# Kernel optimization log

Hardware: AMD Instinct MI355X
Metric: run time of the kernel (lower is better)

Reference implementation:

```python
import jax, jax.numpy as jnp
import numpy as np

B, N, D = 2, 2048, 1024   # batch, seq, input_dim
H, DK, DV = 8, 128, 1024  # heads, qk_dim, v_dim (v_dim == input_dim for residual)


def setup_inputs() -> dict:
    key = jax.random.key(0)
    kx, kq, kk, kv = jax.random.split(key, 4)
    scale = 0.02
    x = jax.random.normal(kx, (B, N, D), dtype=jnp.float32)
    # torch nn.Linear weights are [out_features, in_features]; stacked over heads.
    Wq = jax.random.normal(kq, (H, DK, D), dtype=jnp.float32) * scale
    Wk = jax.random.normal(kk, (H, DK, D), dtype=jnp.float32) * scale
    Wv = jax.random.normal(kv, (H, DV, D), dtype=jnp.float32) * scale
    return {"x": x, "Wq": Wq, "Wk": Wk, "Wv": Wv}


def reference(x, Wq, Wk, Wv):
    # x: [B, N, D]; Wq/Wk: [H, DK, D]; Wv: [H, DV, D]
    n = x.shape[-2]
    Q = jnp.einsum('bnd,hed->bhne', x, Wq)  # [B,H,N,DK]
    K = jnp.einsum('bnd,hed->bhne', x, Wk)  # [B,H,N,DK]
    V = jnp.einsum('bnd,hvd->bhnv', x, Wv)  # [B,H,N,DV]
    scores = jnp.einsum('bhne,bhme->bhnm', Q, K)  # [B,H,N,N]
    # causal mask: masked entries set to mask_value=0.0, then relu, then /N
    causal = jnp.tril(jnp.ones((n, n), dtype=bool))
    sim = jnp.where(causal, jax.nn.relu(scores), jnp.float32(0.0)) / jnp.float32(n)
    # sum of per-head outputs added to residual
    head_out = jnp.einsum('bhnm,bhmv->bnv', sim, V)  # [B,N,DV]
    return x + head_out
```

## Files before the change

kernel.cpp:

```cpp
#include <hip/hip_runtime.h>

typedef __attribute__((ext_vector_type(8))) short bf16x8;
typedef __attribute__((ext_vector_type(4))) float floatx4;

__device__ __forceinline__ unsigned short f2bf(float f) {
  unsigned int u = __builtin_bit_cast(unsigned int, f);
  unsigned int r = (u + 0x7fffu + ((u >> 16) & 1u)) >> 16;
  return (unsigned short)r;
}

__device__ __forceinline__ unsigned int pack2(float a, float b) {
  return (unsigned int)f2bf(a) | ((unsigned int)f2bf(b) << 16);
}

__device__ __forceinline__ void gload16(const void* g, void* l) {
  __builtin_amdgcn_global_load_lds(
      (__attribute__((address_space(1))) void*)g,
      (__attribute__((address_space(3))) void*)l, 16, 0, 0);
}

__device__ __forceinline__ void barrier_lgkm() {
  asm volatile("s_waitcnt lgkmcnt(0)" ::: "memory");
  __builtin_amdgcn_s_barrier();
  __builtin_amdgcn_sched_barrier(0);
}

__global__ __launch_bounds__(256) void init_out(const float4* __restrict__ x,
                                                float4* __restrict__ out, int n4) {
  for (int i = blockIdx.x * 256 + threadIdx.x; i < n4; i += gridDim.x * 256)
    out[i] = x[i];
}

__global__ __launch_bounds__(256) void convert_all(
    const float4* __restrict__ x4,
    const float4* __restrict__ wq4, const float4* __restrict__ wk4,
    const float4* __restrict__ wv4,
    uint2* __restrict__ xb4, uint2* __restrict__ wqkb4, uint2* __restrict__ wvb4)
{
  const int NX = 2 * 2048 * 1024 / 4;
  const int NQK = 8 * 256 * 1024 / 4;
  const int NV = 8 * 1024 * 1024 / 4;
  const int total = NX + NQK + NV;
  const float inv_n = 1.0f / 2048.0f;
  for (int i = blockIdx.x * 256 + threadIdx.x; i < total; i += gridDim.x * 256) {
    float4 f; uint2* dst;
    if (i < NX) {
      f = x4[i]; dst = &xb4[i];
    } else if (i < NX + NQK) {
      int j = i - NX;
      int c = j & 255;
      int row = j >> 8;
      int h = row >> 8, r = row & 255;
      f = (r < 128) ? wq4[(h * 128 + r) * 256 + c] : wk4[(h * 128 + r - 128) * 256 + c];
      dst = &wqkb4[j];
    } else {
      int j = i - NX - NQK;
      f = wv4[j];
      f.x *= inv_n; f.y *= inv_n; f.z *= inv_n; f.w *= inv_n;
      dst = &wvb4[j];
    }
    uint2 p; p.x = pack2(f.x, f.y); p.y = pack2(f.z, f.w);
    *dst = p;
  }
}

__global__ __launch_bounds__(256) void gemm_bf16_bt(
    const unsigned short* __restrict__ Abase, long sAb, long sAh,
    const unsigned short* __restrict__ Bbase, long sBb, long sBh,
    unsigned short* __restrict__ C0base, long sC0, int ld0,
    unsigned short* __restrict__ C1base, long sC1, int ld1,
    int split, int K)
{
  const int z = blockIdx.z;
  const int b = z >> 3, h = z & 7;
  const unsigned short* Ag = Abase + (long)b * sAb + (long)h * sAh + (long)blockIdx.x * 128 * K;
  const unsigned short* Bg = Bbase + (long)b * sBb + (long)h * sBh + (long)blockIdx.y * 128 * K;
  __shared__ __align__(16) unsigned short LA[128 * 64];
  __shared__ __align__(16) unsigned short LB[128 * 64];
  const int t = threadIdx.x;
  const int l = t & 63, w = t >> 6;
  const int wr = w >> 1, wc = w & 1;
  const int l16 = l & 15, lq = l >> 4;
  floatx4 acc[4][4] = {};
  for (int k0 = 0; k0 < K; k0 += 64) {
    __syncthreads();
    for (int i = 0; i < 4; i++) {
      int cbase = i * 256 + (t & 192);
      int chunk = cbase + (t & 63);
      int row = chunk >> 3, c8 = chunk & 7;
      gload16(Ag + (long)row * K + k0 + c8 * 8, &LA[cbase * 8]);
      gload16(Bg + (long)row * K + k0 + c8 * 8, &LB[cbase * 8]);
    }
    __syncthreads();
    for (int kk = 0; kk < 2; kk++) {
      bf16x8 af[4], bfr[4];
      for (int m = 0; m < 4; m++)
        af[m]  = *reinterpret_cast<const bf16x8*>(&LA[(wr * 64 + m * 16 + l16) * 64 + kk * 32 + lq * 8]);
      for (int n = 0; n < 4; n++)
        bfr[n] = *reinterpret_cast<const bf16x8*>(&LB[(wc * 64 + n * 16 + l16) * 64 + kk * 32 + lq * 8]);
      for (int m = 0; m < 4; m++)
        for (int n = 0; n < 4; n++)
          acc[m][n] = __builtin_amdgcn_mfma_f32_16x16x32_bf16(af[m], bfr[n], acc[m][n], 0, 0, 0);
    }
  }
  unsigned short* C0 = C0base + (long)z * sC0;
  unsigned short* C1 = C1base + (long)z * sC1;
  for (int m = 0; m < 4; m++)
    for (int n = 0; n < 4; n++)
      for (int j = 0; j < 4; j++) {
        int row = blockIdx.x * 128 + wr * 64 + m * 16 + lq * 4 + j;
        int col = blockIdx.y * 128 + wc * 64 + n * 16 + l16;
        unsigned short v = f2bf(acc[m][n][j]);
        if (col < split) C0[(long)row * ld0 + col] = v;
        else             C1[(long)row * ld1 + (col - split)] = v;
      }
}

__global__ __launch_bounds__(256) void gemm_bt(
    const float* __restrict__ Abase, long sAb, long sAh,
    const float* __restrict__ Bbase, long sBb, long sBh,
    unsigned short* __restrict__ Cbase, long sC,
    int M, int Nc, int K, int H, float cscale)
{
  int z = blockIdx.z;
  int b = z / H, h = z % H;
  const float* A  = Abase + (long)b * sAb + (long)h * sAh;
  const float* Bm = Bbase + (long)b * sBb + (long)h * sBh;
  unsigned short* C = Cbase + (long)z * sC;
  int tRow = blockIdx.x * 128;
  int tCol = blockIdx.y * 128;
  __shared__ __align__(16) unsigned short LA[128 * 72];
  __shared__ __align__(16) unsigned short LB[128 * 72];
  int t = threadIdx.x;
  int l = t & 63, w = t >> 6;
  int wr = w >> 1, wc = w & 1;
  int l16 = l & 15, lq = l >> 4;
  floatx4 acc[4][4] = {};
  for (int k0 = 0; k0 < K; k0 += 64) {
    __syncthreads();
    for (int i = 0; i < 8; i++) {
      int lin = i * 256 + t;
      int row = lin >> 4;
      int c4  = lin & 15;
      float4 va = *reinterpret_cast<const float4*>(A + (long)(tRow + row) * K + k0 + c4 * 4);
      uint2 pa; pa.x = pack2(va.x, va.y); pa.y = pack2(va.z, va.w);
      *reinterpret_cast<uint2*>(&LA[row * 72 + c4 * 4]) = pa;
      float4 vb = *reinterpret_cast<const float4*>(Bm + (long)(tCol + row) * K + k0 + c4 * 4);
      uint2 pb; pb.x = pack2(vb.x, vb.y); pb.y = pack2(vb.z, vb.w);
      *reinterpret_cast<uint2*>(&LB[row * 72 + c4 * 4]) = pb;
    }
    __syncthreads();
    for (int kk = 0; kk < 2; kk++) {
      bf16x8 af[4], bfr[4];
      for (int m = 0; m < 4; m++)
        af[m]  = *reinterpret_cast<const bf16x8*>(&LA[(wr * 64 + m * 16 + l16) * 72 + kk * 32 + lq * 8]);
      for (int n = 0; n < 4; n++)
        bfr[n] = *reinterpret_cast<const bf16x8*>(&LB[(wc * 64 + n * 16 + l16) * 72 + kk * 32 + lq * 8]);
      for (int m = 0; m < 4; m++)
        for (int n = 0; n < 4; n++)
          acc[m][n] = __builtin_amdgcn_mfma_f32_16x16x32_bf16(af[m], bfr[n], acc[m][n], 0, 0, 0);
    }
  }
  for (int m = 0; m < 4; m++)
    for (int n = 0; n < 4; n++)
      for (int j = 0; j < 4; j++) {
        int row = tRow + wr * 64 + m * 16 + lq * 4 + j;
        int col = tCol + wc * 64 + n * 16 + l16;
        C[(long)row * Nc + col] = f2bf(acc[m][n][j] * cscale);
      }
}

__global__ __launch_bounds__(256) void gemm_qk(
    const float* __restrict__ x,
    const float* __restrict__ Wq, const float* __restrict__ Wk,
    unsigned short* __restrict__ Qb, unsigned short* __restrict__ Kb)
{
  int z = blockIdx.z;
  int b = z >> 3, h = z & 7;
  const float* A  = x + (long)b * 2048 * 1024;
  const float* Bm = (blockIdx.y ? Wk : Wq) + (long)h * 128 * 1024;
  unsigned short* C = (blockIdx.y ? Kb : Qb) + (long)z * 2048 * 128;
  int tRow = blockIdx.x * 128;
  __shared__ __align__(16) unsigned short LA[128 * 72];
  __shared__ __align__(16) unsigned short LB[128 * 72];
  int t = threadIdx.x;
  int l = t & 63, w = t >> 6;
  int wr = w >> 1, wc = w & 1;
  int l16 = l & 15, lq = l >> 4;
  floatx4 acc[4][4] = {};
  const int K = 1024;
  for (int k0 = 0; k0 < K; k0 += 64) {
    __syncthreads();
    for (int i = 0; i < 8; i++) {
      int lin = i * 256 + t;
      int row = lin >> 4;
      int c4  = lin & 15;
      float4 va = *reinterpret_cast<const float4*>(A + (long)(tRow + row) * K + k0 + c4 * 4);
      uint2 pa; pa.x = pack2(va.x, va.y); pa.y = pack2(va.z, va.w);
      *reinterpret_cast<uint2*>(&LA[row * 72 + c4 * 4]) = pa;
      float4 vb = *reinterpret_cast<const float4*>(Bm + (long)row * K + k0 + c4 * 4);
      uint2 pb; pb.x = pack2(vb.x, vb.y); pb.y = pack2(vb.z, vb.w);
      *reinterpret_cast<uint2*>(&LB[row * 72 + c4 * 4]) = pb;
    }
    __syncthreads();
    for (int kk = 0; kk < 2; kk++) {
      bf16x8 af[4], bfr[4];
      for (int m = 0; m < 4; m++)
        af[m]  = *reinterpret_cast<const bf16x8*>(&LA[(wr * 64 + m * 16 + l16) * 72 + kk * 32 + lq * 8]);
      for (int n = 0; n < 4; n++)
        bfr[n] = *reinterpret_cast<const bf16x8*>(&LB[(wc * 64 + n * 16 + l16) * 72 + kk * 32 + lq * 8]);
      for (int m = 0; m < 4; m++)
        for (int n = 0; n < 4; n++)
          acc[m][n] = __builtin_amdgcn_mfma_f32_16x16x32_bf16(af[m], bfr[n], acc[m][n], 0, 0, 0);
    }
  }
  for (int m = 0; m < 4; m++)
    for (int n = 0; n < 4; n++)
      for (int j = 0; j < 4; j++) {
        int row = tRow + wr * 64 + m * 16 + lq * 4 + j;
        int col = wc * 64 + n * 16 + l16;
        C[(long)row * 128 + col] = f2bf(acc[m][n][j]);
      }
}

__global__ __launch_bounds__(256) void attn_fused(
    const unsigned short* __restrict__ Qb,
    const unsigned short* __restrict__ Kb,
    const unsigned short* __restrict__ Vtb,
    float* __restrict__ out)
{
  const int z = blockIdx.z;
  const int b = z >> 3;
  const int pair = blockIdx.y;
  const int vb = blockIdx.x;
  const int t = threadIdx.x;
  const int l = t & 63, w = t >> 6;
  const int l16 = l & 15, lq = l >> 4;
  const int wm = w & 1, wn = w >> 1;
  const int swz = l16 & 7;

  __shared__ __align__(16) unsigned short LK[64 * 128];
  __shared__ __align__(16) unsigned short LV[128 * 64];
  __shared__ __align__(16) unsigned short LP[64 * 64];

  const unsigned short* Qz = Qb + (long)z * 2048 * 128;
  const unsigned short* Kh = Kb + (long)z * 2048 * 128;
  const unsigned short* Vh = Vtb + (long)z * 1024 * 2048 + (long)(vb * 128) * 2048;

  int koff[4], voff[4];
  unsigned short *pK[4], *pV[4];
#pragma unroll
  for (int i = 0; i < 4; i++) {
    int lin = i * 256 + t;
    int r = lin >> 4, c = lin & 15;
    koff[i] = r * 128 + c * 8;
    pK[i] = &LK[r * 128 + ((((c & 7) ^ (r & 7)) | (c & 8)) * 8)];
    int rv = lin >> 3, cv = lin & 7;
    voff[i] = rv * 2048 + cv * 8;
    pV[i] = &LV[rv * 64 + ((cv ^ (rv & 7)) * 8)];
  }

  for (int hf = 0; hf < 2; hf++) {
    const int T = hf ? (31 - pair) : pair;
    const unsigned short* Qh = Qz + (long)T * 64 * 128;
    bf16x8 aQ[2][4];
#pragma unroll
    for (int sn = 0; sn < 2; sn++)
#pragma unroll
      for (int ke = 0; ke < 4; ke++)
        aQ[sn][ke] = *reinterpret_cast<const bf16x8*>(
            Qh + (long)(wn * 32 + sn * 16 + l16) * 128 + ke * 32 + lq * 8);
    floatx4 acc[4][2] = {};
    for (int M = 0; M <= T; M++) {
      uint4 ks[4], vs[4];
#pragma unroll
      for (int i = 0; i < 4; i++) {
        ks[i] = *reinterpret_cast<const uint4*>(Kh + M * 8192 + koff[i]);
        vs[i] = *reinterpret_cast<const uint4*>(Vh + M * 64 + voff[i]);
      }
      barrier_lgkm();
#pragma unroll
      for (int i = 0; i < 4; i++) {
        *reinterpret_cast<uint4*>(pK[i]) = ks[i];
        *reinterpret_cast<uint4*>(pV[i]) = vs[i];
      }
      barrier_lgkm();
      floatx4 sacc[2][2] = {{{}, {}}, {{}, {}}};
      __builtin_amdgcn_s_setprio(1);
#pragma unroll
      for (int ke = 0; ke < 4; ke++) {
        bf16x8 kf[2];
#pragma unroll
        for (int sm = 0; sm < 2; sm++) {
          int chunk = 4 * ke + lq;
          kf[sm] = *reinterpret_cast<const bf16x8*>(
              &LK[(wm * 32 + sm * 16 + l16) * 128 +
                  ((((chunk & 7) ^ swz) | (chunk & 8)) * 8)]);
        }
#pragma unroll
        for (int sm = 0; sm < 2; sm++)
#pragma unroll
          for (int sn = 0; sn < 2; sn++)
            sacc[sm][sn] = __builtin_amdgcn_mfma_f32_16x16x32_bf16(
                kf[sm], aQ[sn][ke], sacc[sm][sn], 0, 0, 0);
      }
      __builtin_amdgcn_s_setprio(0);
      const bool diag = (M == T);
#pragma unroll
      for (int sm = 0; sm < 2; sm++)
#pragma unroll
        for (int sn = 0; sn < 2; sn++) {
          floatx4 v = sacc[sm][sn];
          float f0 = fmaxf(v[0], 0.0f), f1 = fmaxf(v[1], 0.0f);
          float f2 = fmaxf(v[2], 0.0f), f3 = fmaxf(v[3], 0.0f);
          if (diag) {
            int mm = wm * 32 + sm * 16 + lq * 4;
            int nn = wn * 32 + sn * 16 + l16;
            if (mm + 0 > nn) f0 = 0.0f;
            if (mm + 1 > nn) f1 = 0.0f;
            if (mm + 2 > nn) f2 = 0.0f;
            if (mm + 3 > nn) f3 = 0.0f;
          }
          unsigned int p0, p1;
          asm("v_cvt_pk_bf16_f32 %0, %1, %2" : "=v"(p0) : "v"(f0), "v"(f1));
          asm("v_cvt_pk_bf16_f32 %0, %1, %2" : "=v"(p1) : "v"(f2), "v"(f3));
          uint2 pk; pk.x = p0; pk.y = p1;
          int row = wn * 32 + sn * 16 + l16;
          int cs = wm * 32 + sm * 16 + lq * 4;
          *reinterpret_cast<uint2*>(
              &LP[row * 64 + (((cs >> 3) ^ (row & 7)) * 8) + (cs & 7)]) = pk;
        }
      barrier_lgkm();
      __builtin_amdgcn_s_setprio(1);
#pragma unroll
      for (int km = 0; km < 2; km++) {
        bf16x8 aP[4], bV[2];
#pragma unroll
        for (int nf = 0; nf < 4; nf++)
          aP[nf] = *reinterpret_cast<const bf16x8*>(
              &LP[(nf * 16 + l16) * 64 + (((4 * km + lq) ^ swz) * 8)]);
#pragma unroll
        for (int vf = 0; vf < 2; vf++)
          bV[vf] = *reinterpret_cast<const bf16x8*>(
              &LV[(w * 32 + vf * 16 + l16) * 64 + (((4 * km + lq) ^ swz) * 8)]);
#pragma unroll
        for (int nf = 0; nf < 4; nf++)
#pragma unroll
          for (int vf = 0; vf < 2; vf++)
            acc[nf][vf] = __builtin_amdgcn_mfma_f32_16x16x32_bf16(
                aP[nf], bV[vf], acc[nf][vf], 0, 0, 0);
      }
      __builtin_amdgcn_s_setprio(0);
    }
#pragma unroll
    for (int nf = 0; nf < 4; nf++)
#pragma unroll
      for (int vf = 0; vf < 2; vf++)
#pragma unroll
        for (int j = 0; j < 4; j++) {
          int n = T * 64 + nf * 16 + lq * 4 + j;
          int v = vb * 128 + w * 32 + vf * 16 + l16;
          long idx = ((long)b * 2048 + n) * 1024 + v;
          unsafeAtomicAdd(&out[idx], acc[nf][vf][j]);
        }
  }
}

extern "C" void kernel_launch(void* const* d_in, const int* in_sizes, int n_in,
                              void* d_out, int out_size, void* d_ws, size_t ws_size,
                              hipStream_t stream) {
  const float* x  = (const float*)d_in[0];
  const float* Wq = (const float*)d_in[1];
  const float* Wk = (const float*)d_in[2];
  const float* Wv = (const float*)d_in[3];
  float* out = (float*)d_out;
  const size_t MB = 1u << 20;
  dim3 blk(256);

  if (ws_size >= 104 * MB) {
    unsigned short* Vtb  = (unsigned short*)d_ws;
    unsigned short* Wqkb = (unsigned short*)d_ws;
    unsigned short* Qb   = (unsigned short*)((char*)d_ws + 64 * MB);
    unsigned short* Kb   = (unsigned short*)((char*)d_ws + 72 * MB);
    unsigned short* xb   = (unsigned short*)((char*)d_ws + 80 * MB);
    unsigned short* Wvb  = (unsigned short*)((char*)d_ws + 88 * MB);

    convert_all<<<dim3(2048), blk, 0, stream>>>(
        (const float4*)x, (const float4*)Wq, (const float4*)Wk, (const float4*)Wv,
        (uint2*)xb, (uint2*)Wqkb, (uint2*)Wvb);
    init_out<<<dim3(1024), blk, 0, stream>>>(
        (const float4*)x, (float4*)out, 2 * 2048 * 1024 / 4);
    gemm_bf16_bt<<<dim3(16, 2, 16), blk, 0, stream>>>(
        xb, (long)2048 * 1024, 0, Wqkb, 0, (long)256 * 1024,
        Qb, (long)2048 * 128, 128, Kb, (long)2048 * 128, 128, 128, 1024);
    gemm_bf16_bt<<<dim3(8, 16, 16), blk, 0, stream>>>(
        Wvb, 0, (long)1024 * 1024, xb, (long)2048 * 1024, 0,
        Vtb, (long)1024 * 2048, 2048, Vtb, 0, 0, 1 << 30, 1024);
    attn_fused<<<dim3(8, 16, 16), blk, 0, stream>>>(Qb, Kb, Vtb, out);
  } else {
    unsigned short* Qb  = (unsigned short*)d_ws;
    unsigned short* Kb  = Qb + (size_t)2 * 8 * 2048 * 128;
    unsigned short* Vtb = Kb + (size_t)2 * 8 * 2048 * 128;
    init_out<<<dim3(1024), blk, 0, stream>>>(
        (const float4*)x, (float4*)out, 2 * 2048 * 1024 / 4);
    gemm_qk<<<dim3(16, 2, 16), blk, 0, stream>>>(x, Wq, Wk, Qb, Kb);
    gemm_bt<<<dim3(8, 16, 16), blk, 0, stream>>>(
        Wv, 0, (long)1024 * 1024, x, (long)2048 * 1024, 0,
        Vtb, (long)1024 * 2048, 1024, 2048, 1024, 8, 1.0f / 2048.0f);
    attn_fused<<<dim3(8, 16, 16), blk, 0, stream>>>(Qb, Kb, Vtb, out);
  }
}
```

Baseline: 342.1 us.

## Fuse residual copy into convert, merge QK/V GEMMs, widen attention V tile

The residual copy of x into out moves into the conversion kernel, and the Q/K and V projection GEMMs become a single launch with a flat block index. The attention kernel now covers 256 V columns per block instead of 128, which halves the number of blocks that recompute the QK scores. V fragments are read straight from global memory into registers rather than staged through LDS. This cuts launches and redundant score work, at the cost of more accumulator registers and uncoalesced direct global V loads that may expose latency.

```diff
diff --git a/kernel.cpp b/kernel.cpp
--- a/kernel.cpp
+++ b/kernel.cpp
@@ -25,17 +25,12 @@
   __builtin_amdgcn_sched_barrier(0);
 }
 
-__global__ __launch_bounds__(256) void init_out(const float4* __restrict__ x,
-                                                float4* __restrict__ out, int n4) {
-  for (int i = blockIdx.x * 256 + threadIdx.x; i < n4; i += gridDim.x * 256)
-    out[i] = x[i];
-}
-
 __global__ __launch_bounds__(256) void convert_all(
     const float4* __restrict__ x4,
     const float4* __restrict__ wq4, const float4* __restrict__ wk4,
     const float4* __restrict__ wv4,
-    uint2* __restrict__ xb4, uint2* __restrict__ wqkb4, uint2* __restrict__ wvb4)
+    uint2* __restrict__ xb4, uint2* __restrict__ wqkb4, uint2* __restrict__ wvb4,
+    float4* __restrict__ out4)
 {
   const int NX = 2 * 2048 * 1024 / 4;
   const int NQK = 8 * 256 * 1024 / 4;
@@ -46,6 +41,7 @@
     float4 f; uint2* dst;
     if (i < NX) {
       f = x4[i]; dst = &xb4[i];
+      out4[i] = f;
     } else if (i < NX + NQK) {
       int j = i - NX;
       int c = j & 255;
@@ -64,32 +60,30 @@
   }
 }
 
-__global__ __launch_bounds__(256) void gemm_bf16_bt(
-    const unsigned short* __restrict__ Abase, long sAb, long sAh,
-    const unsigned short* __restrict__ Bbase, long sBb, long sBh,
-    unsigned short* __restrict__ C0base, long sC0, int ld0,
-    unsigned short* __restrict__ C1base, long sC1, int ld1,
-    int split, int K)
-{
-  const int z = blockIdx.z;
-  const int b = z >> 3, h = z & 7;
-  const unsigned short* Ag = Abase + (long)b * sAb + (long)h * sAh + (long)blockIdx.x * 128 * K;
-  const unsigned short* Bg = Bbase + (long)b * sBb + (long)h * sBh + (long)blockIdx.y * 128 * K;
-  __shared__ __align__(16) unsigned short LA[128 * 64];
-  __shared__ __align__(16) unsigned short LB[128 * 64];
-  const int t = threadIdx.x;
+__global__ __launch_bounds__(256) void init_out(const float4* __restrict__ x,
+                                                float4* __restrict__ out, int n4) {
+  for (int i = blockIdx.x * 256 + threadIdx.x; i < n4; i += gridDim.x * 256)
+    out[i] = x[i];
+}
+
+__device__ __forceinline__ void gemm_body(
+    const unsigned short* __restrict__ Ag,
+    const unsigned short* __restrict__ Bg,
+    unsigned short* __restrict__ C, long ld,
+    unsigned short* LA, unsigned short* LB, int t)
+{
   const int l = t & 63, w = t >> 6;
   const int wr = w >> 1, wc = w & 1;
   const int l16 = l & 15, lq = l >> 4;
   floatx4 acc[4][4] = {};
-  for (int k0 = 0; k0 < K; k0 += 64) {
+  for (int k0 = 0; k0 < 1024; k0 += 64) {
     __syncthreads();
     for (int i = 0; i < 4; i++) {
       int cbase = i * 256 + (t & 192);
       int chunk = cbase + (t & 63);
       int row = chunk >> 3, c8 = chunk & 7;
-      gload16(Ag + (long)row * K + k0 + c8 * 8, &LA[cbase * 8]);
-      gload16(Bg + (long)row * K + k0 + c8 * 8, &LB[cbase * 8]);
+      gload16(Ag + (long)row * 1024 + k0 + c8 * 8, &LA[cbase * 8]);
+      gload16(Bg + (long)row * 1024 + k0 + c8 * 8, &LB[cbase * 8]);
     }
     __syncthreads();
     for (int kk = 0; kk < 2; kk++) {
@@ -103,17 +97,42 @@
           acc[m][n] = __builtin_amdgcn_mfma_f32_16x16x32_bf16(af[m], bfr[n], acc[m][n], 0, 0, 0);
     }
   }
-  unsigned short* C0 = C0base + (long)z * sC0;
-  unsigned short* C1 = C1base + (long)z * sC1;
   for (int m = 0; m < 4; m++)
     for (int n = 0; n < 4; n++)
       for (int j = 0; j < 4; j++) {
-        int row = blockIdx.x * 128 + wr * 64 + m * 16 + lq * 4 + j;
-        int col = blockIdx.y * 128 + wc * 64 + n * 16 + l16;
-        unsigned short v = f2bf(acc[m][n][j]);
-        if (col < split) C0[(long)row * ld0 + col] = v;
-        else             C1[(long)row * ld1 + (col - split)] = v;
+        int row = wr * 64 + m * 16 + lq * 4 + j;
+        int col = wc * 64 + n * 16 + l16;
+        C[(long)row * ld + col] = f2bf(acc[m][n][j]);
       }
+}
+
+__global__ __launch_bounds__(256) void gemm_all(
+    const unsigned short* __restrict__ xb,
+    const unsigned short* __restrict__ Wqkb,
+    const unsigned short* __restrict__ Wvb,
+    unsigned short* __restrict__ Qb, unsigned short* __restrict__ Kb,
+    unsigned short* __restrict__ Vtb)
+{
+  __shared__ __align__(16) unsigned short LA[128 * 64];
+  __shared__ __align__(16) unsigned short LB[128 * 64];
+  const int bid = blockIdx.x;
+  const int t = threadIdx.x;
+  if (bid < 512) {
+    int bx = bid & 15, qy = (bid >> 4) & 1, z = bid >> 5;
+    int b = z >> 3, h = z & 7;
+    const unsigned short* Ag = xb + (long)b * 2048 * 1024 + (long)bx * 128 * 1024;
+    const unsigned short* Bg = Wqkb + (long)h * 256 * 1024 + (long)qy * 128 * 1024;
+    unsigned short* C = (qy ? Kb : Qb) + (long)z * 2048 * 128 + (long)bx * 128 * 128;
+    gemm_body(Ag, Bg, C, 128, LA, LB, t);
+  } else {
+    int v = bid - 512;
+    int bx = v & 7, by = (v >> 3) & 15, z = v >> 7;
+    int b = z >> 3, h = z & 7;
+    const unsigned short* Ag = Wvb + (long)h * 1024 * 1024 + (long)bx * 128 * 1024;
+    const unsigned short* Bg = xb + (long)b * 2048 * 1024 + (long)by * 128 * 1024;
+    unsigned short* C = Vtb + (long)z * 1024 * 2048 + (long)bx * 128 * 2048 + by * 128;
+    gemm_body(Ag, Bg, C, 2048, LA, LB, t);
+  }
 }
 
 __global__ __launch_bounds__(256) void gemm_bt(
@@ -240,24 +259,20 @@
   const int swz = l16 & 7;
 
   __shared__ __align__(16) unsigned short LK[64 * 128];
-  __shared__ __align__(16) unsigned short LV[128 * 64];
   __shared__ __align__(16) unsigned short LP[64 * 64];
 
   const unsigned short* Qz = Qb + (long)z * 2048 * 128;
   const unsigned short* Kh = Kb + (long)z * 2048 * 128;
-  const unsigned short* Vh = Vtb + (long)z * 1024 * 2048 + (long)(vb * 128) * 2048;
-
-  int koff[4], voff[4];
-  unsigned short *pK[4], *pV[4];
+  const unsigned short* Vw = Vtb + (long)z * 1024 * 2048 +
+                             (long)(vb * 256 + w * 64 + l16) * 2048;
+
+  int koff[4]; unsigned short* pK[4];
 #pragma unroll
   for (int i = 0; i < 4; i++) {
     int lin = i * 256 + t;
     int r = lin >> 4, c = lin & 15;
     koff[i] = r * 128 + c * 8;
     pK[i] = &LK[r * 128 + ((((c & 7) ^ (r & 7)) | (c & 8)) * 8)];
-    int rv = lin >> 3, cv = lin & 7;
-    voff[i] = rv * 2048 + cv * 8;
-    pV[i] = &LV[rv * 64 + ((cv ^ (rv & 7)) * 8)];
   }
 
   for (int hf = 0; hf < 2; hf++) {
@@ -270,20 +285,16 @@
       for (int ke = 0; ke < 4; ke++)
         aQ[sn][ke] = *reinterpret_cast<const bf16x8*>(
             Qh + (long)(wn * 32 + sn * 16 + l16) * 128 + ke * 32 + lq * 8);
-    floatx4 acc[4][2] = {};
+    floatx4 acc[4][4] = {};
     for (int M = 0; M <= T; M++) {
-      uint4 ks[4], vs[4];
-#pragma unroll
-      for (int i = 0; i < 4; i++) {
+      uint4 ks[4];
+#pragma unroll
+      for (int i = 0; i < 4; i++)
         ks[i] = *reinterpret_cast<const uint4*>(Kh + M * 8192 + koff[i]);
-        vs[i] = *reinterpret_cast<const uint4*>(Vh + M * 64 + voff[i]);
-      }
       barrier_lgkm();
 #pragma unroll
-      for (int i = 0; i < 4; i++) {
+      for (int i = 0; i < 4; i++)
         *reinterpret_cast<uint4*>(pK[i]) = ks[i];
-        *reinterpret_cast<uint4*>(pV[i]) = vs[i];
-      }
       barrier_lgkm();
       floatx4 sacc[2][2] = {{{}, {}}, {{}, {}}};
       __builtin_amdgcn_s_setprio(1);
@@ -330,36 +341,52 @@
           *reinterpret_cast<uint2*>(
               &LP[row * 64 + (((cs >> 3) ^ (row & 7)) * 8) + (cs & 7)]) = pk;
         }
+      bf16x8 bv0[4];
+#pragma unroll
+      for (int vf = 0; vf < 4; vf++)
+        bv0[vf] = *reinterpret_cast<const bf16x8*>(
+            Vw + (long)(vf * 16) * 2048 + M * 64 + lq * 8);
       barrier_lgkm();
       __builtin_amdgcn_s_setprio(1);
-#pragma unroll
-      for (int km = 0; km < 2; km++) {
-        bf16x8 aP[4], bV[2];
+      {
+        bf16x8 aP[4];
 #pragma unroll
         for (int nf = 0; nf < 4; nf++)
           aP[nf] = *reinterpret_cast<const bf16x8*>(
-              &LP[(nf * 16 + l16) * 64 + (((4 * km + lq) ^ swz) * 8)]);
-#pragma unroll
-        for (int vf = 0; vf < 2; vf++)
-          bV[vf] = *reinterpret_cast<const bf16x8*>(
-              &LV[(w * 32 + vf * 16 + l16) * 64 + (((4 * km + lq) ^ swz) * 8)]);
+              &LP[(nf * 16 + l16) * 64 + ((lq ^ swz) * 8)]);
+        bf16x8 bv1[4];
+#pragma unroll
+        for (int vf = 0; vf < 4; vf++)
+          bv1[vf] = *reinterpret_cast<const bf16x8*>(
+              Vw + (long)(vf * 16) * 2048 + M * 64 + 32 + lq * 8);
 #pragma unroll
         for (int nf = 0; nf < 4; nf++)
 #pragma unroll
-          for (int vf = 0; vf < 2; vf++)
+          for (int vf = 0; vf < 4; vf++)
             acc[nf][vf] = __builtin_amdgcn_mfma_f32_16x16x32_bf16(
-                aP[nf], bV[vf], acc[nf][vf], 0, 0, 0);
+                aP[nf], bv0[vf], acc[nf][vf], 0, 0, 0);
+        bf16x8 aP1[4];
+#pragma unroll
+        for (int nf = 0; nf < 4; nf++)
+          aP1[nf] = *reinterpret_cast<const bf16x8*>(
+              &LP[(nf * 16 + l16) * 64 + (((4 + lq) ^ swz) * 8)]);
+#pragma unroll
+        for (int nf = 0; nf < 4; nf++)
+#pragma unroll
+          for (int vf = 0; vf < 4; vf++)
+            acc[nf][vf] = __builtin_amdgcn_mfma_f32_16x16x32_bf16(
+                aP1[nf], bv1[vf], acc[nf][vf], 0, 0, 0);
       }
       __builtin_amdgcn_s_setprio(0);
     }
 #pragma unroll
     for (int nf = 0; nf < 4; nf++)
 #pragma unroll
-      for (int vf = 0; vf < 2; vf++)
+      for (int vf = 0; vf < 4; vf++)
 #pragma unroll
         for (int j = 0; j < 4; j++) {
           int n = T * 64 + nf * 16 + lq * 4 + j;
-          int v = vb * 128 + w * 32 + vf * 16 + l16;
+          int v = vb * 256 + w * 64 + vf * 16 + l16;
           long idx = ((long)b * 2048 + n) * 1024 + v;
           unsafeAtomicAdd(&out[idx], acc[nf][vf][j]);
         }
@@ -387,16 +414,9 @@
 
     convert_all<<<dim3(2048), blk, 0, stream>>>(
         (const float4*)x, (const float4*)Wq, (const float4*)Wk, (const float4*)Wv,
-        (uint2*)xb, (uint2*)Wqkb, (uint2*)Wvb);
-    init_out<<<dim3(1024), blk, 0, stream>>>(
-        (const float4*)x, (float4*)out, 2 * 2048 * 1024 / 4);
-    gemm_bf16_bt<<<dim3(16, 2, 16), blk, 0, stream>>>(
-        xb, (long)2048 * 1024, 0, Wqkb, 0, (long)256 * 1024,
-        Qb, (long)2048 * 128, 128, Kb, (long)2048 * 128, 128, 128, 1024);
-    gemm_bf16_bt<<<dim3(8, 16, 16), blk, 0, stream>>>(
-        Wvb, 0, (long)1024 * 1024, xb, (long)2048 * 1024, 0,
-        Vtb, (long)1024 * 2048, 2048, Vtb, 0, 0, 1 << 30, 1024);
-    attn_fused<<<dim3(8, 16, 16), blk, 0, stream>>>(Qb, Kb, Vtb, out);
+        (uint2*)xb, (uint2*)Wqkb, (uint2*)Wvb, (float4*)out);
+    gemm_all<<<dim3(2560), blk, 0, stream>>>(xb, Wqkb, Wvb, Qb, Kb, Vtb);
+    attn_fused<<<dim3(4, 16, 16), blk, 0, stream>>>(Qb, Kb, Vtb, out);
   } else {
     unsigned short* Qb  = (unsigned short*)d_ws;
     unsigned short* Kb  = Qb + (size_t)2 * 8 * 2048 * 128;
@@ -407,6 +427,6 @@
     gemm_bt<<<dim3(8, 16, 16), blk, 0, stream>>>(
         Wv, 0, (long)1024 * 1024, x, (long)2048 * 1024, 0,
         Vtb, (long)1024 * 2048, 1024, 2048, 1024, 8, 1.0f / 2048.0f);
-    attn_fused<<<dim3(8, 16, 16), blk, 0, stream>>>(Qb, Kb, Vtb, out);
-  }
-}
+    attn_fused<<<dim3(4, 16, 16), blk, 0, stream>>>(Qb, Kb, Vtb, out);
+  }
+}
```

Result: slower. 361.5 us (+5.7%).
